# Kernel optimization log

Hardware: AMD Instinct MI355X
Metric: run time of the kernel (lower is better)

Reference implementation:

```python
import jax, jax.numpy as jnp
import numpy as np

N = 100000
E = 1600000
IN_C, HID, OUT_C = 500, 256, 40
K, ALPHA = 10, 0.1
LN_EPS = 1e-5


def setup_inputs() -> dict:
    key = jax.random.key(0)
    ks = jax.random.split(key, 12)
    glorot = lambda k, i, o: jax.random.normal(k, (i, o), jnp.float32) * (1.0 / np.sqrt(i))
    return {
        "x": jax.random.normal(ks[0], (N, IN_C), jnp.float32),
        "edge_index": jax.random.randint(ks[1], (2, E), 0, N, jnp.int64),
        "W1": glorot(ks[2], IN_C, HID), "b1": jnp.zeros((HID,), jnp.float32),
        "g1": jnp.ones((HID,), jnp.float32), "be1": jnp.zeros((HID,), jnp.float32),
        "W2": glorot(ks[3], HID, HID), "b2": jnp.zeros((HID,), jnp.float32),
        "g2": jnp.ones((HID,), jnp.float32), "be2": jnp.zeros((HID,), jnp.float32),
        "W3": glorot(ks[4], HID, OUT_C), "b3": jnp.zeros((OUT_C,), jnp.float32),
    }


def _layernorm(h, g, b):
    mu = jnp.mean(h, axis=-1, keepdims=True)
    var = jnp.mean(jnp.square(h - mu), axis=-1, keepdims=True)
    return (h - mu) * jax.lax.rsqrt(var + LN_EPS) * g + b


def reference(x, edge_index, W1, b1, g1, be1, W2, b2, g2, be2, W3, b3):
    # --- MLP (eval mode: dropout inactive) ---
    h = _layernorm(jax.nn.gelu(x @ W1 + b1, approximate=False), g1, be1)
    h = _layernorm(jax.nn.gelu(h @ W2 + b2, approximate=False), g2, be2)
    h = h @ W3 + b3  # [N, OUT_C]

    # --- GCN normalization with self-loops (PyG gcn_norm) ---
    loops = jnp.arange(N, dtype=edge_index.dtype)
    row = jnp.concatenate([edge_index[0], loops])  # source
    col = jnp.concatenate([edge_index[1], loops])  # target
    deg = jax.ops.segment_sum(jnp.ones_like(col, jnp.float32), col, num_segments=N)
    dinv = jnp.where(deg > 0, jax.lax.rsqrt(deg), 0.0)
    norm = dinv[row] * dinv[col]  # [E+N]

    # --- APPNP: K steps of h <- (1-alpha) * A_hat h + alpha * h0 ---
    h0 = h
    for _ in range(K):
        msg = norm[:, None] * h[row]                       # gather + scale
        agg = jax.ops.segment_sum(msg, col, num_segments=N)  # scatter-add
        h = (1.0 - ALPHA) * agg + ALPHA * h0
    return h
```

## Files before the change

kernel.cpp:

```cpp
#include <hip/hip_runtime.h>
#include <hip/hip_bf16.h>
#include <math.h>

#define N_NODES 100000
#define N_EDGES 1600000
#define IN_C    500
#define HID     256
#define OUT_C   40
#define K_ITERS 10
#define ALPHA   0.1f
#define LN_EPS  1e-5f

#define K1PAD   512
#define K2PAD   256

#define SCAN_CHUNK 1024
#define NBLK_SCAN  ((N_NODES + SCAN_CHUNK - 1) / SCAN_CHUNK)

typedef __attribute__((ext_vector_type(8))) short bf16x8;
typedef __attribute__((ext_vector_type(4))) float f32x4;

__device__ __forceinline__ void split2(float a, short& hi, short& lo) {
    const unsigned ua = __float_as_uint(a);
    hi = (short)(ua >> 16);
    const float r = a - __uint_as_float(ua & 0xffff0000u);
    lo = (short)(__float_as_uint(r) >> 16);
}

__device__ __forceinline__ void async_load16(const void* g, void* l) {
    __builtin_amdgcn_global_load_lds(
        (const __attribute__((address_space(1))) void*)g,
        (__attribute__((address_space(3))) void*)l, 16, 0, 0);
}

__global__ void deg_count_kernel(const int* __restrict__ col, int* __restrict__ cnt, int e) {
    int i = blockIdx.x * blockDim.x + threadIdx.x;
    if (i < e) atomicAdd(&cnt[col[i]], 1);
}

__global__ void dinv_kernel(const int* __restrict__ cnt, float* __restrict__ dinv, int n) {
    int i = blockIdx.x * blockDim.x + threadIdx.x;
    if (i < n) dinv[i] = rsqrtf((float)cnt[i] + 1.0f);
}

__global__ __launch_bounds__(256) void scan_partial_kernel(const int* __restrict__ cnt,
                                                           int* __restrict__ bsum) {
    __shared__ int s[256];
    const int base = blockIdx.x * SCAN_CHUNK;
    const int t = threadIdx.x;
    int sum = 0;
    #pragma unroll
    for (int j = 0; j < 4; j++) {
        int idx = base + t * 4 + j;
        if (idx < N_NODES) sum += cnt[idx];
    }
    s[t] = sum;
    __syncthreads();
    for (int off = 128; off > 0; off >>= 1) {
        if (t < off) s[t] += s[t + off];
        __syncthreads();
    }
    if (t == 0) bsum[blockIdx.x] = s[0];
}

__global__ __launch_bounds__(128) void scan_bsum_kernel(int* __restrict__ bsum, int nblk) {
    __shared__ int s[128];
    const int t = threadIdx.x;
    const int orig = (t < nblk) ? bsum[t] : 0;
    s[t] = orig;
    __syncthreads();
    for (int off = 1; off < 128; off <<= 1) {
        int v = 0;
        if (t >= off) v = s[t - off];
        __syncthreads();
        s[t] += v;
        __syncthreads();
    }
    if (t < nblk) bsum[t] = s[t] - orig;
}

__global__ __launch_bounds__(256) void scan_final_kernel(const int* __restrict__ cnt,
                                                         const int* __restrict__ bsum,
                                                         int* __restrict__ offs) {
    __shared__ int s[256];
    const int base = blockIdx.x * SCAN_CHUNK;
    const int t = threadIdx.x;
    int v[4];
    int lsum = 0;
    #pragma unroll
    for (int j = 0; j < 4; j++) {
        int idx = base + t * 4 + j;
        v[j] = (idx < N_NODES) ? cnt[idx] : 0;
        lsum += v[j];
    }
    s[t] = lsum;
    __syncthreads();
    const int orig = lsum;
    for (int off = 1; off < 256; off <<= 1) {
        int u = 0;
        if (t >= off) u = s[t - off];
        __syncthreads();
        s[t] += u;
        __syncthreads();
    }
    int run = bsum[blockIdx.x] + (s[t] - orig);
    #pragma unroll
    for (int j = 0; j < 4; j++) {
        int idx = base + t * 4 + j;
        if (idx < N_NODES) offs[idx] = run;
        run += v[j];
    }
}

__global__ void set_total_kernel(int* __restrict__ offs) {
    if (threadIdx.x == 0 && blockIdx.x == 0) offs[N_NODES] = N_EDGES;
}

__global__ void csr_fill_kernel(const int* __restrict__ row, const int* __restrict__ col,
                                const float* __restrict__ dinv, const int* __restrict__ offs,
                                int* __restrict__ cursor, int2* __restrict__ csr_ew, int e) {
    int i = blockIdx.x * blockDim.x + threadIdx.x;
    if (i >= e) return;
    const int r = row[i], c = col[i];
    const int p = offs[c] + atomicAdd(&cursor[c], 1);
    csr_ew[p] = make_int2(r, __float_as_int(dinv[r] * dinv[c]));
}

__global__ __launch_bounds__(256) void wsplit_kernel(
    const float* __restrict__ W, short* __restrict__ hi, short* __restrict__ lo,
    int K, int Nn, int Kpad)
{
    const int idx = blockIdx.x * 256 + threadIdx.x;
    if (idx >= Nn * Kpad) return;
    const int n = idx / Kpad, k = idx - n * Kpad;
    const float v = (k < K) ? W[(size_t)k * Nn + n] : 0.0f;
    short h, l;
    split2(v, h, l);
    hi[idx] = h;
    lo[idx] = l;
}

#define GBM 64
#define GBN 256
#define GBK 32

__global__ __launch_bounds__(256) void gemm1_fused_kernel(
    const float* __restrict__ X,
    const short* __restrict__ Bhi, const short* __restrict__ Blo,
    const float* __restrict__ bias, float* __restrict__ C, int M)
{
    __shared__ short As[2][GBM * GBK];
    __shared__ short Bs[2][GBN * GBK];

    const int tid  = threadIdx.x;
    const int wid  = tid >> 6, lane = tid & 63;
    const int wm   = wid >> 1, wn = wid & 1;
    const int fm   = lane & 15, fq = lane >> 4;
    const int row0 = blockIdx.x * GBM;

    const int ar   = tid >> 2;
    const int aseg = tid & 3;
    const int gr   = min(row0 + ar, M - 1);

    f32x4 acc[2][8] = {};

    for (int ks = 0; ks < K1PAD / GBK; ks++) {
        const int k0 = ks * GBK;
        __syncthreads();

        #pragma unroll
        for (int i = 0; i < 4; i++) {
            const int c  = i * 256 + tid;
            const int n  = c >> 2, k8 = (c & 3) * 8;
            const int cb = (i * 256 + wid * 64) * 8;
            const size_t oB = (size_t)n * K1PAD + k0 + k8;
            async_load16(Bhi + oB, &Bs[0][cb]);
            async_load16(Blo + oB, &Bs[1][cb]);
        }
        {
            const int kb = k0 + aseg * 8;
            float v[8];
            if (k0 + GBK <= IN_C) {
                const float4 v0 = *(const float4*)(X + (size_t)gr * IN_C + kb);
                const float4 v1 = *(const float4*)(X + (size_t)gr * IN_C + kb + 4);
                v[0]=v0.x; v[1]=v0.y; v[2]=v0.z; v[3]=v0.w;
                v[4]=v1.x; v[5]=v1.y; v[6]=v1.z; v[7]=v1.w;
            } else {
                #pragma unroll
                for (int j = 0; j < 8; j++)
                    v[j] = (kb + j < IN_C) ? X[(size_t)gr * IN_C + kb + j] : 0.0f;
            }
            bf16x8 h8, l8;
            #pragma unroll
            for (int j = 0; j < 8; j++) { short th, tl; split2(v[j], th, tl); h8[j] = th; l8[j] = tl; }
            *(bf16x8*)&As[0][ar * GBK + aseg * 8] = h8;
            *(bf16x8*)&As[1][ar * GBK + aseg * 8] = l8;
        }
        __syncthreads();

        bf16x8 ah[2], al[2];
        #pragma unroll
        for (int tm = 0; tm < 2; tm++) {
            const int r = wm * 32 + tm * 16 + fm;
            ah[tm] = *(const bf16x8*)&As[0][r * GBK + fq * 8];
            al[tm] = *(const bf16x8*)&As[1][r * GBK + fq * 8];
        }
        #pragma unroll
        for (int tn = 0; tn < 8; tn++) {
            const int cc = wn * 128 + tn * 16 + fm;
            const bf16x8 bh = *(const bf16x8*)&Bs[0][cc * GBK + fq * 8];
            const bf16x8 bl = *(const bf16x8*)&Bs[1][cc * GBK + fq * 8];
            #pragma unroll
            for (int tm = 0; tm < 2; tm++) {
                acc[tm][tn] = __builtin_amdgcn_mfma_f32_16x16x32_bf16(ah[tm], bh, acc[tm][tn], 0, 0, 0);
                acc[tm][tn] = __builtin_amdgcn_mfma_f32_16x16x32_bf16(ah[tm], bl, acc[tm][tn], 0, 0, 0);
                acc[tm][tn] = __builtin_amdgcn_mfma_f32_16x16x32_bf16(al[tm], bh, acc[tm][tn], 0, 0, 0);
            }
        }
    }

    #pragma unroll
    for (int tm = 0; tm < 2; tm++) {
        #pragma unroll
        for (int tn = 0; tn < 8; tn++) {
            const int gc = wn * 128 + tn * 16 + fm;
            const float bv = bias[gc];
            #pragma unroll
            for (int r = 0; r < 4; r++) {
                const int gr2 = row0 + wm * 32 + tm * 16 + fq * 4 + r;
                if (gr2 < M) {
                    float v = acc[tm][tn][r] + bv;
                    v = 0.5f * v * (1.0f + erff(v * 0.70710678118654752f));
                    C[(size_t)gr2 * 256 + gc] = v;
                }
            }
        }
    }
}

__global__ __launch_bounds__(256) void gemm2_kernel(
    const short* __restrict__ Ahi, const short* __restrict__ Alo,
    const short* __restrict__ Bhi, const short* __restrict__ Blo,
    const float* __restrict__ bias, float* __restrict__ C, int M)
{
    __shared__ short As[2][GBM * GBK];
    __shared__ short Bs[2][GBN * GBK];

    const int tid  = threadIdx.x;
    const int wid  = tid >> 6, lane = tid & 63;
    const int wm   = wid >> 1, wn = wid & 1;
    const int fm   = lane & 15, fq = lane >> 4;
    const int row0 = blockIdx.x * GBM;

    f32x4 acc[2][8] = {};

    for (int ks = 0; ks < K2PAD / GBK; ks++) {
        const int k0 = ks * GBK;
        __syncthreads();

        #pragma unroll
        for (int i = 0; i < 4; i++) {
            const int c  = i * 256 + tid;
            const int n  = c >> 2, k8 = (c & 3) * 8;
            const int cb = (i * 256 + wid * 64) * 8;
            const size_t oB = (size_t)n * K2PAD + k0 + k8;
            async_load16(Bhi + oB, &Bs[0][cb]);
            async_load16(Blo + oB, &Bs[1][cb]);
        }
        {
            const int m  = tid >> 2, k8 = (tid & 3) * 8;
            const int cb = (wid * 64) * 8;
            const size_t oA = (size_t)min(row0 + m, M - 1) * K2PAD + k0 + k8;
            async_load16(Ahi + oA, &As[0][cb]);
            async_load16(Alo + oA, &As[1][cb]);
        }
        __syncthreads();

        bf16x8 ah[2], al[2];
        #pragma unroll
        for (int tm = 0; tm < 2; tm++) {
            const int r = wm * 32 + tm * 16 + fm;
            ah[tm] = *(const bf16x8*)&As[0][r * GBK + fq * 8];
            al[tm] = *(const bf16x8*)&As[1][r * GBK + fq * 8];
        }
        #pragma unroll
        for (int tn = 0; tn < 8; tn++) {
            const int cc = wn * 128 + tn * 16 + fm;
            const bf16x8 bh = *(const bf16x8*)&Bs[0][cc * GBK + fq * 8];
            const bf16x8 bl = *(const bf16x8*)&Bs[1][cc * GBK + fq * 8];
            #pragma unroll
            for (int tm = 0; tm < 2; tm++) {
                acc[tm][tn] = __builtin_amdgcn_mfma_f32_16x16x32_bf16(ah[tm], bh, acc[tm][tn], 0, 0, 0);
                acc[tm][tn] = __builtin_amdgcn_mfma_f32_16x16x32_bf16(ah[tm], bl, acc[tm][tn], 0, 0, 0);
                acc[tm][tn] = __builtin_amdgcn_mfma_f32_16x16x32_bf16(al[tm], bh, acc[tm][tn], 0, 0, 0);
            }
        }
    }

    #pragma unroll
    for (int tm = 0; tm < 2; tm++) {
        #pragma unroll
        for (int tn = 0; tn < 8; tn++) {
            const int gc = wn * 128 + tn * 16 + fm;
            const float bv = bias[gc];
            #pragma unroll
            for (int r = 0; r < 4; r++) {
                const int gr2 = row0 + wm * 32 + tm * 16 + fq * 4 + r;
                if (gr2 < M) {
                    float v = acc[tm][tn][r] + bv;
                    v = 0.5f * v * (1.0f + erff(v * 0.70710678118654752f));
                    C[(size_t)gr2 * 256 + gc] = v;
                }
            }
        }
    }
}

__global__ __launch_bounds__(256) void layernorm_split_kernel(
    const float* __restrict__ h, const float* __restrict__ g, const float* __restrict__ b,
    short* __restrict__ hi, short* __restrict__ lo, int nrows)
{
    const int wave = threadIdx.x >> 6;
    const int lane = threadIdx.x & 63;
    const int row  = blockIdx.x * 4 + wave;
    if (row >= nrows) return;

    const float* p = h + (size_t)row * HID;
    float v[4];
    float s = 0.0f;
    #pragma unroll
    for (int j = 0; j < 4; j++) { v[j] = p[lane + 64 * j]; s += v[j]; }
    #pragma unroll
    for (int off = 32; off > 0; off >>= 1) s += __shfl_xor(s, off);
    const float mu = s * (1.0f / 256.0f);

    float vs = 0.0f;
    #pragma unroll
    for (int j = 0; j < 4; j++) { float d = v[j] - mu; vs += d * d; }
    #pragma unroll
    for (int off = 32; off > 0; off >>= 1) vs += __shfl_xor(vs, off);
    const float rs = rsqrtf(vs * (1.0f / 256.0f) + LN_EPS);

    #pragma unroll
    for (int j = 0; j < 4; j++) {
        const int c = lane + 64 * j;
        const float o = (v[j] - mu) * rs * g[c] + b[c];
        short th, tl;
        split2(o, th, tl);
        hi[(size_t)row * HID + c] = th;
        lo[(size_t)row * HID + c] = tl;
    }
}

__global__ __launch_bounds__(256) void layernorm_kernel(
    float* __restrict__ h, const float* __restrict__ g, const float* __restrict__ b, int nrows)
{
    const int wave = threadIdx.x >> 6;
    const int lane = threadIdx.x & 63;
    const int row  = blockIdx.x * 4 + wave;
    if (row >= nrows) return;

    float* p = h + (size_t)row * HID;
    float v[4];
    float s = 0.0f;
    #pragma unroll
    for (int j = 0; j < 4; j++) { v[j] = p[lane + 64 * j]; s += v[j]; }
    #pragma unroll
    for (int off = 32; off > 0; off >>= 1) s += __shfl_xor(s, off);
    const float mu = s * (1.0f / 256.0f);

    float vs = 0.0f;
    #pragma unroll
    for (int j = 0; j < 4; j++) { float d = v[j] - mu; vs += d * d; }
    #pragma unroll
    for (int off = 32; off > 0; off >>= 1) vs += __shfl_xor(vs, off);
    const float rs = rsqrtf(vs * (1.0f / 256.0f) + LN_EPS);

    #pragma unroll
    for (int j = 0; j < 4; j++) {
        int c = lane + 64 * j;
        p[c] = (v[j] - mu) * rs * g[c] + b[c];
    }
}

__global__ __launch_bounds__(256) void gemm3_kernel(
    const float* __restrict__ A, const float* __restrict__ W,
    const float* __restrict__ bias, float* __restrict__ C, int M)
{
    __shared__ float Ws[HID * OUT_C];
    __shared__ float bs[OUT_C];
    for (int i = threadIdx.x; i < HID * OUT_C; i += 256) Ws[i] = W[i];
    if (threadIdx.x < OUT_C) bs[threadIdx.x] = bias[threadIdx.x];
    __syncthreads();

    const int total = M * OUT_C;
    for (int idx = blockIdx.x * 256 + threadIdx.x; idx < total; idx += gridDim.x * 256) {
        const int r = idx / OUT_C;
        const int c = idx - r * OUT_C;
        const float4* a4 = reinterpret_cast<const float4*>(A + (size_t)r * HID);
        float s = 0.0f;
        #pragma unroll 4
        for (int k4 = 0; k4 < HID / 4; k4++) {
            float4 av = a4[k4];
            const float* wp = &Ws[k4 * 4 * OUT_C + c];
            s += av.x * wp[0] + av.y * wp[OUT_C] + av.z * wp[2 * OUT_C] + av.w * wp[3 * OUT_C];
        }
        C[idx] = s + bs[c];
    }
}

__global__ __launch_bounds__(256) void appnp_kernel(
    const int* __restrict__ offs, const int2* __restrict__ csr_ew,
    const float* __restrict__ dinv,
    const float* __restrict__ h, const float* __restrict__ h0,
    float* __restrict__ out)
{
    const int node = blockIdx.x * 4 + (threadIdx.x >> 6);
    if (node >= N_NODES) return;
    const int lane = threadIdx.x & 63;
    const int g = lane / 10;
    const int q = lane - g * 10;
    const bool act = (lane < 60);

    const int start = offs[node];
    const int end   = offs[node + 1];

    float ax = 0.0f, ay = 0.0f, az = 0.0f, aw = 0.0f;
    for (int e0 = start; e0 < end; e0 += 6) {
        const int  ee = e0 + g;
        const bool ea = act && (ee < end);
        const int2 ed = csr_ew[ea ? ee : start];
        const float w = ea ? __int_as_float(ed.y) : 0.0f;
        const float4 hv = *(const float4*)(h + (size_t)ed.x * OUT_C + q * 4);
        ax += w * hv.x; ay += w * hv.y; az += w * hv.z; aw += w * hv.w;
    }

    ax += __shfl(ax, lane + 30); ay += __shfl(ay, lane + 30);
    az += __shfl(az, lane + 30); aw += __shfl(aw, lane + 30);
    {
        const float bx = __shfl(ax, lane + 10), cx = __shfl(ax, lane + 20);
        const float by = __shfl(ay, lane + 10), cy = __shfl(ay, lane + 20);
        const float bz = __shfl(az, lane + 10), cz = __shfl(az, lane + 20);
        const float bw = __shfl(aw, lane + 10), cw = __shfl(aw, lane + 20);
        ax += bx + cx; ay += by + cy; az += bz + cz; aw += bw + cw;
    }

    if (lane < 10) {
        const float d = dinv[node];
        const float self = d * d;
        const size_t idx = (size_t)node * OUT_C + lane * 4;
        const float4 hs  = *(const float4*)(h + idx);
        const float4 h0v = *(const float4*)(h0 + idx);
        float4 o;
        o.x = (1.0f - ALPHA) * (ax + self * hs.x) + ALPHA * h0v.x;
        o.y = (1.0f - ALPHA) * (ay + self * hs.y) + ALPHA * h0v.y;
        o.z = (1.0f - ALPHA) * (az + self * hs.z) + ALPHA * h0v.z;
        o.w = (1.0f - ALPHA) * (aw + self * hs.w) + ALPHA * h0v.w;
        *(float4*)(out + idx) = o;
    }
}

extern "C" void kernel_launch(void* const* d_in, const int* in_sizes, int n_in,
                              void* d_out, int out_size, void* d_ws, size_t ws_size,
                              hipStream_t stream) {
    const float* x   = (const float*)d_in[0];
    const int*   ei  = (const int*)d_in[1];
    const float* W1  = (const float*)d_in[2];
    const float* b1  = (const float*)d_in[3];
    const float* g1  = (const float*)d_in[4];
    const float* be1 = (const float*)d_in[5];
    const float* W2  = (const float*)d_in[6];
    const float* b2  = (const float*)d_in[7];
    const float* g2  = (const float*)d_in[8];
    const float* be2 = (const float*)d_in[9];
    const float* W3  = (const float*)d_in[10];
    const float* b3  = (const float*)d_in[11];
    float* out = (float*)d_out;

    const int* e_row = ei;
    const int* e_col = ei + N_EDGES;

    float* ws = (float*)d_ws;
    size_t off = 0;
    float* dinv = ws + off; off += N_NODES;
    int*   cnt  = (int*)(ws + off); off += N_NODES;
    int*   offs = (int*)(ws + off); off += N_NODES + 1;
    int*   bsum = (int*)(ws + off); off += 128 + 3;
    short* W1hi = (short*)(ws + off); off += 65536;
    short* W1lo = (short*)(ws + off); off += 65536;
    short* W2hi = (short*)(ws + off); off += 32768;
    short* W2lo = (short*)(ws + off); off += 32768;
    float* t1 = ws + off; off += (size_t)N_NODES * HID;
    float* t2 = t1;
    float* regA = ws + off; off += (size_t)N_NODES * HID;
    short* A2hi = (short*)regA;
    short* A2lo = A2hi + (size_t)N_NODES * HID;
    int2*  csr_ew = (int2*)regA;
    float* h0 = regA + 2 * (size_t)N_EDGES;
    float* hA = h0 + (size_t)N_NODES * OUT_C;
    float* hB = hA + (size_t)N_NODES * OUT_C;

    hipMemsetAsync(cnt, 0, N_NODES * sizeof(int), stream);
    deg_count_kernel<<<(N_EDGES + 255) / 256, 256, 0, stream>>>(e_col, cnt, N_EDGES);
    dinv_kernel<<<(N_NODES + 255) / 256, 256, 0, stream>>>(cnt, dinv, N_NODES);
    scan_partial_kernel<<<NBLK_SCAN, 256, 0, stream>>>(cnt, bsum);
    scan_bsum_kernel<<<1, 128, 0, stream>>>(bsum, NBLK_SCAN);
    scan_final_kernel<<<NBLK_SCAN, 256, 0, stream>>>(cnt, bsum, offs);
    set_total_kernel<<<1, 64, 0, stream>>>(offs);

    wsplit_kernel<<<(256 * K1PAD + 255) / 256, 256, 0, stream>>>(W1, W1hi, W1lo, IN_C, 256, K1PAD);
    wsplit_kernel<<<(256 * K2PAD + 255) / 256, 256, 0, stream>>>(W2, W2hi, W2lo, HID, 256, K2PAD);

    {
        const int nblk = (N_NODES + GBM - 1) / GBM;
        gemm1_fused_kernel<<<nblk, 256, 0, stream>>>(x, W1hi, W1lo, b1, t1, N_NODES);
        layernorm_split_kernel<<<(N_NODES + 3) / 4, 256, 0, stream>>>(t1, g1, be1, A2hi, A2lo, N_NODES);
        gemm2_kernel<<<nblk, 256, 0, stream>>>(A2hi, A2lo, W2hi, W2lo, b2, t2, N_NODES);
        layernorm_kernel<<<(N_NODES + 3) / 4, 256, 0, stream>>>(t2, g2, be2, N_NODES);
        gemm3_kernel<<<2048, 256, 0, stream>>>(t2, W3, b3, h0, N_NODES);
    }

    hipMemsetAsync(cnt, 0, N_NODES * sizeof(int), stream);
    csr_fill_kernel<<<(N_EDGES + 255) / 256, 256, 0, stream>>>(
        e_row, e_col, dinv, offs, cnt, csr_ew, N_EDGES);

    const float* hcur = h0;
    for (int it = 0; it < K_ITERS; it++) {
        float* tgt = (it == K_ITERS - 1) ? out : ((it & 1) ? hB : hA);
        appnp_kernel<<<(N_NODES + 3) / 4, 256, 0, stream>>>(
            offs, csr_ew, dinv, hcur, h0, tgt);
        hcur = tgt;
    }
}
```

Before: 1.580 ms.

## Double-buffer GEMM shared-memory tiles with XOR swizzle and register prefetch

Both MLP GEMM kernels now use two shared-memory buffers, so the async loads for the next K-slice are issued before computing on the current one, and only one barrier is needed per step. gemm1 also prefetches X into registers two steps ahead. An XOR swizzle on the k-segment index is meant to cut LDS bank conflicts on the MFMA fragment reads, and launch bounds request two blocks per CU. The cost is twice the LDS (about 80KB per block) and more register pressure, which may limit occupancy; the GEMMs are only part of a runtime dominated by the sparse propagation.

New measurement: 1.573 ms. About the same (-0.5%).

```diff
diff --git a/kernel.cpp b/kernel.cpp
--- a/kernel.cpp
+++ b/kernel.cpp
@@ -143,14 +143,16 @@
 #define GBM 64
 #define GBN 256
 #define GBK 32
-
-__global__ __launch_bounds__(256) void gemm1_fused_kernel(
+#define NSTEP1 (K1PAD / GBK)
+#define NSTEP2 (K2PAD / GBK)
+
+__global__ __launch_bounds__(256, 2) void gemm1_fused_kernel(
     const float* __restrict__ X,
     const short* __restrict__ Bhi, const short* __restrict__ Blo,
     const float* __restrict__ bias, float* __restrict__ C, int M)
 {
-    __shared__ short As[2][GBM * GBK];
-    __shared__ short Bs[2][GBN * GBK];
+    __shared__ short As[2][2][GBM * GBK];
+    __shared__ short Bs[2][2][GBN * GBK];
 
     const int tid  = threadIdx.x;
     const int wid  = tid >> 6, lane = tid & 63;
@@ -161,61 +163,87 @@
     const int ar   = tid >> 2;
     const int aseg = tid & 3;
     const int gr   = min(row0 + ar, M - 1);
+    const int asw  = (aseg ^ ((ar >> 1) & 3)) * 8;
 
     f32x4 acc[2][8] = {};
 
-    for (int ks = 0; ks < K1PAD / GBK; ks++) {
+    auto stageB = [&](int ks, int buf) {
         const int k0 = ks * GBK;
-        __syncthreads();
-
         #pragma unroll
         for (int i = 0; i < 4; i++) {
             const int c  = i * 256 + tid;
-            const int n  = c >> 2, k8 = (c & 3) * 8;
+            const int n  = c >> 2;
+            const int k8 = ((c & 3) ^ ((n >> 1) & 3)) * 8;
             const int cb = (i * 256 + wid * 64) * 8;
             const size_t oB = (size_t)n * K1PAD + k0 + k8;
-            async_load16(Bhi + oB, &Bs[0][cb]);
-            async_load16(Blo + oB, &Bs[1][cb]);
-        }
-        {
-            const int kb = k0 + aseg * 8;
-            float v[8];
-            if (k0 + GBK <= IN_C) {
-                const float4 v0 = *(const float4*)(X + (size_t)gr * IN_C + kb);
-                const float4 v1 = *(const float4*)(X + (size_t)gr * IN_C + kb + 4);
-                v[0]=v0.x; v[1]=v0.y; v[2]=v0.z; v[3]=v0.w;
-                v[4]=v1.x; v[5]=v1.y; v[6]=v1.z; v[7]=v1.w;
-            } else {
-                #pragma unroll
-                for (int j = 0; j < 8; j++)
-                    v[j] = (kb + j < IN_C) ? X[(size_t)gr * IN_C + kb + j] : 0.0f;
-            }
-            bf16x8 h8, l8;
+            async_load16(Bhi + oB, &Bs[buf][0][cb]);
+            async_load16(Blo + oB, &Bs[buf][1][cb]);
+        }
+    };
+    auto loadX = [&](int ks, float* v) {
+        const int kb = ks * GBK + aseg * 8;
+        if (kb + 8 <= IN_C) {
+            const float4 v0 = *(const float4*)(X + (size_t)gr * IN_C + kb);
+            const float4 v1 = *(const float4*)(X + (size_t)gr * IN_C + kb + 4);
+            v[0]=v0.x; v[1]=v0.y; v[2]=v0.z; v[3]=v0.w;
+            v[4]=v1.x; v[5]=v1.y; v[6]=v1.z; v[7]=v1.w;
+        } else {
             #pragma unroll
-            for (int j = 0; j < 8; j++) { short th, tl; split2(v[j], th, tl); h8[j] = th; l8[j] = tl; }
-            *(bf16x8*)&As[0][ar * GBK + aseg * 8] = h8;
-            *(bf16x8*)&As[1][ar * GBK + aseg * 8] = l8;
-        }
-        __syncthreads();
-
+            for (int j = 0; j < 8; j++)
+                v[j] = (kb + j < IN_C) ? X[(size_t)gr * IN_C + kb + j] : 0.0f;
+        }
+    };
+    auto writeA = [&](const float* v, int buf) {
+        bf16x8 h8, l8;
+        #pragma unroll
+        for (int j = 0; j < 8; j++) { short th, tl; split2(v[j], th, tl); h8[j] = th; l8[j] = tl; }
+        *(bf16x8*)&As[buf][0][ar * GBK + asw] = h8;
+        *(bf16x8*)&As[buf][1][ar * GBK + asw] = l8;
+    };
+    auto compute = [&](int buf) {
         bf16x8 ah[2], al[2];
         #pragma unroll
         for (int tm = 0; tm < 2; tm++) {
-            const int r = wm * 32 + tm * 16 + fm;
-            ah[tm] = *(const bf16x8*)&As[0][r * GBK + fq * 8];
-            al[tm] = *(const bf16x8*)&As[1][r * GBK + fq * 8];
+            const int r   = wm * 32 + tm * 16 + fm;
+            const int ks8 = (fq ^ ((r >> 1) & 3)) * 8;
+            ah[tm] = *(const bf16x8*)&As[buf][0][r * GBK + ks8];
+            al[tm] = *(const bf16x8*)&As[buf][1][r * GBK + ks8];
         }
         #pragma unroll
         for (int tn = 0; tn < 8; tn++) {
-            const int cc = wn * 128 + tn * 16 + fm;
-            const bf16x8 bh = *(const bf16x8*)&Bs[0][cc * GBK + fq * 8];
-            const bf16x8 bl = *(const bf16x8*)&Bs[1][cc * GBK + fq * 8];
+            const int cc  = wn * 128 + tn * 16 + fm;
+            const int ks8 = (fq ^ ((cc >> 1) & 3)) * 8;
+            const bf16x8 bh = *(const bf16x8*)&Bs[buf][0][cc * GBK + ks8];
+            const bf16x8 bl = *(const bf16x8*)&Bs[buf][1][cc * GBK + ks8];
             #pragma unroll
             for (int tm = 0; tm < 2; tm++) {
                 acc[tm][tn] = __builtin_amdgcn_mfma_f32_16x16x32_bf16(ah[tm], bh, acc[tm][tn], 0, 0, 0);
                 acc[tm][tn] = __builtin_amdgcn_mfma_f32_16x16x32_bf16(ah[tm], bl, acc[tm][tn], 0, 0, 0);
                 acc[tm][tn] = __builtin_amdgcn_mfma_f32_16x16x32_bf16(al[tm], bh, acc[tm][tn], 0, 0, 0);
             }
+        }
+    };
+
+    float xvA[8], xvB[8];
+    loadX(0, xvA);
+    stageB(0, 0);
+    loadX(1, xvB);
+    writeA(xvA, 0);
+    __syncthreads();
+
+    #pragma unroll
+    for (int ks = 0; ks < NSTEP1; ks += 2) {
+        if (ks + 1 < NSTEP1) stageB(ks + 1, 1);
+        if (ks + 2 < NSTEP1) loadX(ks + 2, xvA);
+        compute(0);
+        if (ks + 1 < NSTEP1) writeA(xvB, 1);
+        __syncthreads();
+        if (ks + 1 < NSTEP1) {
+            if (ks + 2 < NSTEP1) stageB(ks + 2, 0);
+            if (ks + 3 < NSTEP1) loadX(ks + 3, xvB);
+            compute(1);
+            if (ks + 2 < NSTEP1) writeA(xvA, 0);
+            __syncthreads();
         }
     }
 
@@ -238,13 +266,13 @@
     }
 }
 
-__global__ __launch_bounds__(256) void gemm2_kernel(
+__global__ __launch_bounds__(256, 2) void gemm2_kernel(
     const short* __restrict__ Ahi, const short* __restrict__ Alo,
     const short* __restrict__ Bhi, const short* __restrict__ Blo,
     const float* __restrict__ bias, float* __restrict__ C, int M)
 {
-    __shared__ short As[2][GBM * GBK];
-    __shared__ short Bs[2][GBN * GBK];
+    __shared__ short As[2][2][GBM * GBK];
+    __shared__ short Bs[2][2][GBN * GBK];
 
     const int tid  = threadIdx.x;
     const int wid  = tid >> 6, lane = tid & 63;
@@ -254,46 +282,63 @@
 
     f32x4 acc[2][8] = {};
 
-    for (int ks = 0; ks < K2PAD / GBK; ks++) {
+    auto stage = [&](int ks, int buf) {
         const int k0 = ks * GBK;
-        __syncthreads();
-
+        {
+            const int m  = tid >> 2;
+            const int k8 = ((tid & 3) ^ ((m >> 1) & 3)) * 8;
+            const int cb = (wid * 64) * 8;
+            const size_t oA = (size_t)min(row0 + m, M - 1) * K2PAD + k0 + k8;
+            async_load16(Ahi + oA, &As[buf][0][cb]);
+            async_load16(Alo + oA, &As[buf][1][cb]);
+        }
         #pragma unroll
         for (int i = 0; i < 4; i++) {
             const int c  = i * 256 + tid;
-            const int n  = c >> 2, k8 = (c & 3) * 8;
+            const int n  = c >> 2;
+            const int k8 = ((c & 3) ^ ((n >> 1) & 3)) * 8;
             const int cb = (i * 256 + wid * 64) * 8;
             const size_t oB = (size_t)n * K2PAD + k0 + k8;
-            async_load16(Bhi + oB, &Bs[0][cb]);
-            async_load16(Blo + oB, &Bs[1][cb]);
-        }
-        {
-            const int m  = tid >> 2, k8 = (tid & 3) * 8;
-            const int cb = (wid * 64) * 8;
-            const size_t oA = (size_t)min(row0 + m, M - 1) * K2PAD + k0 + k8;
-            async_load16(Ahi + oA, &As[0][cb]);
-            async_load16(Alo + oA, &As[1][cb]);
-        }
-        __syncthreads();
-
+            async_load16(Bhi + oB, &Bs[buf][0][cb]);
+            async_load16(Blo + oB, &Bs[buf][1][cb]);
+        }
+    };
+    auto compute = [&](int buf) {
         bf16x8 ah[2], al[2];
         #pragma unroll
         for (int tm = 0; tm < 2; tm++) {
-            const int r = wm * 32 + tm * 16 + fm;
-            ah[tm] = *(const bf16x8*)&As[0][r * GBK + fq * 8];
-            al[tm] = *(const bf16x8*)&As[1][r * GBK + fq * 8];
+            const int r   = wm * 32 + tm * 16 + fm;
+            const int ks8 = (fq ^ ((r >> 1) & 3)) * 8;
+            ah[tm] = *(const bf16x8*)&As[buf][0][r * GBK + ks8];
+            al[tm] = *(const bf16x8*)&As[buf][1][r * GBK + ks8];
         }
         #pragma unroll
         for (int tn = 0; tn < 8; tn++) {
-            const int cc = wn * 128 + tn * 16 + fm;
-            const bf16x8 bh = *(const bf16x8*)&Bs[0][cc * GBK + fq * 8];
-            const bf16x8 bl = *(const bf16x8*)&Bs[1][cc * GBK + fq * 8];
+            const int cc  = wn * 128 + tn * 16 + fm;
+            const int ks8 = (fq ^ ((cc >> 1) & 3)) * 8;
+            const bf16x8 bh = *(const bf16x8*)&Bs[buf][0][cc * GBK + ks8];
+            const bf16x8 bl = *(const bf16x8*)&Bs[buf][1][cc * GBK + ks8];
             #pragma unroll
             for (int tm = 0; tm < 2; tm++) {
                 acc[tm][tn] = __builtin_amdgcn_mfma_f32_16x16x32_bf16(ah[tm], bh, acc[tm][tn], 0, 0, 0);
                 acc[tm][tn] = __builtin_amdgcn_mfma_f32_16x16x32_bf16(ah[tm], bl, acc[tm][tn], 0, 0, 0);
                 acc[tm][tn] = __builtin_amdgcn_mfma_f32_16x16x32_bf16(al[tm], bh, acc[tm][tn], 0, 0, 0);
             }
+        }
+    };
+
+    stage(0, 0);
+    __syncthreads();
+
+    #pragma unroll
+    for (int ks = 0; ks < NSTEP2; ks += 2) {
+        if (ks + 1 < NSTEP2) stage(ks + 1, 1);
+        compute(0);
+        __syncthreads();
+        if (ks + 1 < NSTEP2) {
+            if (ks + 2 < NSTEP2) stage(ks + 2, 0);
+            compute(1);
+            __syncthreads();
         }
     }
 
```
